# Optimization experiments

Measured on AMD Instinct MI355X. Metric: run time of the kernel, lower is better.

The kernel has to match this reference:

```python
import jax, jax.numpy as jnp
import numpy as np

B, L, D = 2, 4096, 1024      # batch, seq_len, d_model (expand_ratio=1 -> d_inner == D)
DS, RK, K = 16, 64, 3        # d_state, dt_rank, conv kernel size
EPS = 1e-5


def setup_inputs() -> dict:
    key = jax.random.key(0)
    ks = jax.random.split(key, 16)
    s = 0.02
    inp = {
        "x":      jax.random.normal(ks[0], (B, L, D), jnp.float32),
        "gamma":  jnp.ones((D,), jnp.float32),
        "beta":   jnp.zeros((D,), jnp.float32),
        "W_in":   jax.random.normal(ks[1], (D, 2 * D), jnp.float32) * s,
        "conv_w": jax.random.normal(ks[2], (K, 1, D), jnp.float32) * s,   # depthwise (k, 1, d)
        "conv_b": jnp.zeros((D,), jnp.float32),
        "W_xp":   jax.random.normal(ks[3], (D, RK), jnp.float32) * s,
        "W_Bg":   jax.random.normal(ks[4], (D, DS), jnp.float32) * s,
        "W_Cg":   jax.random.normal(ks[5], (D, DS), jnp.float32) * s,
        "W_dt":   jax.random.normal(ks[6], (RK, D), jnp.float32) * s,
        "b_dt":   jnp.zeros((D,), jnp.float32),
        "W_Bp":   jax.random.normal(ks[7], (DS, D), jnp.float32) * s,
        "W_Cp":   jax.random.normal(ks[8], (DS, D), jnp.float32) * s,
        "A":      -jnp.exp(jax.random.normal(ks[9], (D,), jnp.float32) * 0.5),  # negative for stability
        "D_skip": jnp.ones((D,), jnp.float32),
        "W_out":  jax.random.normal(ks[10], (D, D), jnp.float32) * s,
    }
    return inp


def reference(x, gamma, beta, W_in, conv_w, conv_b, W_xp, W_Bg, W_Cg,
              W_dt, b_dt, W_Bp, W_Cp, A, D_skip, W_out):
    d = x.shape[-1]
    # 1. LayerNorm
    mu = jnp.mean(x, -1, keepdims=True)
    var = jnp.mean(jnp.square(x - mu), -1, keepdims=True)
    xn = (x - mu) * jax.lax.rsqrt(var + EPS) * gamma + beta
    # 2. in_proj + split into main/gate branch
    xz = xn @ W_in                                 # (b, l, 2d)
    xb, z = jnp.split(xz, 2, axis=-1)
    # 3. depthwise Conv1D (same padding) + SiLU
    xc = jax.lax.conv_general_dilated(
        xb, conv_w, window_strides=(1,), padding='SAME',
        dimension_numbers=('NWC', 'WIO', 'NWC'), feature_group_count=d) + conv_b
    x_act = jax.nn.silu(xc)                        # (b, l, d)
    # SSM parameter generation
    delta = jax.nn.softplus((x_act @ W_xp) @ W_dt + b_dt)   # (b, l, d)
    Bm = (x_act @ W_Bg) @ W_Bp                     # (b, l, d)
    Cm = (x_act @ W_Cg) @ W_Cp                     # (b, l, d)
    # 4. diagonal selective scan: h_t = exp(delta*A)*h_{t-1} + delta*B*x ; y = C*h
    dA = jnp.exp(delta * A)
    dBx = delta * Bm * x_act
    def step(h, ab):
        a, bx = ab
        h = a * h + bx
        return h, h
    h0 = jnp.zeros_like(dA[:, 0])
    _, hs = jax.lax.scan(step, h0, (dA.transpose(1, 0, 2), dBx.transpose(1, 0, 2)))
    y = Cm * hs.transpose(1, 0, 2)
    # 5. skip-D, gating, out_proj + residual
    out_ssm = y + x_act * D_skip
    gated = out_ssm * jax.nn.silu(z)
    return gated @ W_out + x
```

## Files before the change

kernel.cpp:

```cpp
#include <hip/hip_runtime.h>
#include <math.h>

#define BB 2
#define LL 4096
#define DD 1024
#define DS 16
#define RK 64
#define MM (BB*LL)
#define NC 128
#define LC (LL/NC)

typedef __attribute__((ext_vector_type(8))) short short8;
typedef __attribute__((ext_vector_type(4))) float f32x4;

__device__ __forceinline__ unsigned short f2bf(float f) {
    union { float f; unsigned u; } v; v.f = f;
    unsigned r = v.u + 0x7fff + ((v.u >> 16) & 1);
    return (unsigned short)(r >> 16);
}
__device__ __forceinline__ float bf2f(unsigned short u) {
    union { unsigned u; float f; } v; v.u = ((unsigned)u) << 16;
    return v.f;
}
__device__ __forceinline__ float2 bf2x2(unsigned u) {
    return make_float2(bf2f((unsigned short)u), bf2f((unsigned short)(u >> 16)));
}
__device__ __forceinline__ unsigned f2bfx2(float lo, float hi) {
    return (unsigned)f2bf(lo) | ((unsigned)f2bf(hi) << 16);
}
__device__ __forceinline__ float fast_rcp(float x) {
    return __builtin_amdgcn_rcpf(x);
}
__device__ __forceinline__ float silu_f(float v) {
    return v * fast_rcp(1.0f + __expf(-v));
}
__device__ __forceinline__ void gload16(const void* g, void* l) {
    __builtin_amdgcn_global_load_lds(
        (const __attribute__((address_space(1))) unsigned int*)g,
        (__attribute__((address_space(3))) unsigned int*)l, 16, 0, 0);
}

__global__ __launch_bounds__(256)
void prep_misc(const float* __restrict__ W_in, const float* __restrict__ W_out,
               const float* __restrict__ W_xp, const float* __restrict__ W_Bg,
               const float* __restrict__ W_Cg, const float* __restrict__ W_dt,
               const float* __restrict__ W_Bp, const float* __restrict__ W_Cp,
               unsigned short* __restrict__ WinT, unsigned short* __restrict__ WoutT,
               unsigned short* __restrict__ WgT, unsigned short* __restrict__ WdtT,
               float* __restrict__ WBpT, float* __restrict__ WCpT,
               const float* __restrict__ x, const float* __restrict__ gamma,
               const float* __restrict__ beta, unsigned short* __restrict__ xn_bf) {
    __shared__ float t[32][33];
    __shared__ float ss[4], qq[4];
    int b = blockIdx.x;
    if (b >= 4224) {
        int row = b - 4224;
        int tid = threadIdx.x;
        const float4* xr = (const float4*)(x + (size_t)row * DD);
        float4 v = xr[tid];
        float s = v.x + v.y + v.z + v.w;
        float q = v.x*v.x + v.y*v.y + v.z*v.z + v.w*v.w;
        #pragma unroll
        for (int off = 32; off > 0; off >>= 1) {
            s += __shfl_down(s, off);
            q += __shfl_down(q, off);
        }
        int wv = tid >> 6;
        if ((tid & 63) == 0) { ss[wv] = s; qq[wv] = q; }
        __syncthreads();
        float S = ss[0] + ss[1] + ss[2] + ss[3];
        float Q = qq[0] + qq[1] + qq[2] + qq[3];
        float mu  = S * (1.0f / DD);
        float var = Q * (1.0f / DD) - mu * mu;
        float r = rsqrtf(var + 1e-5f);
        int d0 = tid * 4;
        float4 gv = *(const float4*)(gamma + d0);
        float4 bv = *(const float4*)(beta + d0);
        ushort4 o;
        o.x = f2bf((v.x - mu) * r * gv.x + bv.x);
        o.y = f2bf((v.y - mu) * r * gv.y + bv.y);
        o.z = f2bf((v.z - mu) * r * gv.z + bv.z);
        o.w = f2bf((v.w - mu) * r * gv.w + bv.w);
        *(ushort4*)&xn_bf[(size_t)row * DD + d0] = o;
    } else if (b < 3072) {
        const float* W; unsigned short* WT; int K, N, n0, k0;
        if (b < 2048) { W = W_in;  WT = WinT;  K = DD; N = 2 * DD;
                        n0 = (b & 63) * 32; k0 = (b >> 6) * 32; }
        else { int bb = b - 2048; W = W_out; WT = WoutT; K = DD; N = DD;
               n0 = (bb & 31) * 32; k0 = (bb >> 5) * 32; }
        int tx = threadIdx.x & 31, ty = threadIdx.x >> 5;
        #pragma unroll
        for (int r = 0; r < 32; r += 8)
            t[ty + r][tx] = W[(size_t)(k0 + ty + r) * N + n0 + tx];
        __syncthreads();
        #pragma unroll
        for (int r = 0; r < 32; r += 8) {
            int nl = ty + r;
            WT[(size_t)(n0 + nl) * K + k0 + tx] = f2bf(t[tx][nl]);
        }
    } else if (b < 3584) {
        int idx = (b - 3072) * 256 + threadIdx.x;
        int k = idx & 1023, n = idx >> 10;
        float v = 0.0f;
        if (n < 64)       v = W_xp[k * RK + n];
        else if (n < 80)  v = W_Bg[k * DS + (n - 64)];
        else if (n < 96)  v = W_Cg[k * DS + (n - 80)];
        WgT[idx] = f2bf(v);
    } else if (b < 4096) {
        int idx = (b - 3584) * 256 + threadIdx.x;
        int k = idx & 127, n = idx >> 7;
        float v = (k < 64) ? W_dt[k * 1024 + n] : 0.0f;
        WdtT[idx] = f2bf(v);
    } else if (b < 4160) {
        int idx = (b - 4096) * 256 + threadIdx.x;
        WBpT[idx] = W_Bp[(idx & 15) * 1024 + (idx >> 4)];
    } else {
        int idx = (b - 4160) * 256 + threadIdx.x;
        WCpT[idx] = W_Cp[(idx & 15) * 1024 + (idx >> 4)];
    }
}

#define MF(a, b, c) __builtin_amdgcn_mfma_f32_16x16x32_bf16(a, b, c, 0, 0, 0)
template<int EPI, int BM>
__global__ __launch_bounds__(512, 1)
void gemm256(const unsigned short* __restrict__ A, const unsigned short* __restrict__ BT,
             void* __restrict__ C0v, void* __restrict__ C1v,
             const float* __restrict__ res, int M, int N, int K) {
    constexpr int MR = BM / 32;
    constexpr int RA = BM / 64;
    constexpr int ABUF = BM * 64;
    extern __shared__ unsigned short sm[];
    unsigned short* As = sm;
    unsigned short* Bs = sm + 2 * ABUF;
    const int tid = threadIdx.x;
    const int wave = tid >> 6, lane = tid & 63;
    const int wr = wave >> 2, wc = wave & 3;
    const int fr = lane & 15, fs = lane >> 4;

    int nbx = gridDim.x;
    int nwg = nbx * gridDim.y;
    int bid = blockIdx.y * nbx + blockIdx.x;
    int cpx = nwg >> 3;
    int swz = (bid & 7) * cpx + (bid >> 3);
    int by = swz / nbx, bx = swz - by * nbx;
    size_t rb = (size_t)by * BM, cb = (size_t)bx * 256;

    const int srow = tid >> 3;
    const int ssw  = (tid & 7) ^ (srow & 7);
    const unsigned short* gA = A + (rb + srow) * K + ssw * 8;
    const unsigned short* gB = BT + (cb + srow) * K + ssw * 8;
    const size_t rstep = (size_t)64 * K;
    unsigned short* dA = As + tid * 8;
    unsigned short* dB = Bs + tid * 8;
    const int T = K >> 6;

#define STGA(rnd, buf, kt) gload16(gA + (size_t)(rnd) * rstep + (size_t)(kt) * 64, dA + (buf) * ABUF + (rnd) * 4096)
#define STGB(rnd, buf, kt) gload16(gB + (size_t)(rnd) * rstep + (size_t)(kt) * 64, dB + (buf) * 16384 + (rnd) * 4096)
#define FOFF(r, S) (((r) << 6) + ((((S) ^ ((r) & 7))) << 3))
#define LDA(i, kk) (*(const short8*)&Ab[FOFF(arow0 + ((i) << 4), fs + ((kk) << 2))])
#define LDB(j, kk) (*(const short8*)&Bb[FOFF(brow0 + ((j) << 4), fs + ((kk) << 2))])

    const int arow0 = wr * (BM / 2) + fr;
    const int brow0 = wc * 64 + fr;

    f32x4 acc[MR][4] = {};

    #pragma unroll
    for (int r = 0; r < RA; ++r) STGA(r, 0, 0);
    #pragma unroll
    for (int r = 0; r < 4; ++r) STGB(r, 0, 0);

    #pragma unroll 1
    for (int t = 0; t < T; ++t) {
        const int cur = t & 1, nx = cur ^ 1;
        const bool pf = (t + 1) < T;
        const unsigned short* Ab = As + cur * ABUF;
        const unsigned short* Bb = Bs + cur * 16384;

        if (pf) { STGA(0, nx, t + 1); STGB(0, nx, t + 1); }
        if (pf) { asm volatile("s_waitcnt vmcnt(2)" ::: "memory"); }
        else    { asm volatile("s_waitcnt vmcnt(0)" ::: "memory"); }
        __builtin_amdgcn_s_barrier();
        __builtin_amdgcn_sched_barrier(0);

        short8 bfr[4][2];
        #pragma unroll
        for (int j = 0; j < 4; ++j) {
            bfr[j][0] = LDB(j, 0);
            bfr[j][1] = LDB(j, 1);
        }
        __builtin_amdgcn_s_setprio(1);
        #pragma unroll
        for (int ii = 0; ii < MR / 4; ++ii) {
            short8 a0 = LDA(ii, 0), a1 = LDA(ii, 1);
            #pragma unroll
            for (int j = 0; j < 4; ++j) {
                acc[ii][j] = MF(a0, bfr[j][0], acc[ii][j]);
                acc[ii][j] = MF(a1, bfr[j][1], acc[ii][j]);
            }
        }
        __builtin_amdgcn_s_setprio(0);
        __builtin_amdgcn_sched_barrier(0);

        #pragma unroll
        for (int p = 1; p < 4; ++p) {
            if (pf) {
                if (p < RA) STGA(p, nx, t + 1);
                STGB(p, nx, t + 1);
            }
            __builtin_amdgcn_s_setprio(1);
            #pragma unroll
            for (int ii = 0; ii < MR / 4; ++ii) {
                const int i = p * (MR / 4) + ii;
                short8 a0 = LDA(i, 0), a1 = LDA(i, 1);
                #pragma unroll
                for (int j = 0; j < 4; ++j) {
                    acc[i][j] = MF(a0, bfr[j][0], acc[i][j]);
                    acc[i][j] = MF(a1, bfr[j][1], acc[i][j]);
                }
            }
            __builtin_amdgcn_s_setprio(0);
            __builtin_amdgcn_sched_barrier(0);
        }
        __builtin_amdgcn_s_barrier();
    }

    const int row0 = (int)rb + wr * (BM / 2) + fs * 4;
    const int col0 = (int)cb + wc * 64 + fr;
    if (EPI == 1) {
        unsigned short* Cd = (cb < DD) ? (unsigned short*)C0v : (unsigned short*)C1v;
        const int cadj = (cb < DD) ? 0 : -DD;
        #pragma unroll
        for (int i = 0; i < MR; ++i)
            #pragma unroll
            for (int j = 0; j < 4; ++j) {
                int col = col0 + cadj + (j << 4);
                #pragma unroll
                for (int q = 0; q < 4; ++q)
                    Cd[(size_t)(row0 + (i << 4) + q) * DD + col] = f2bf(acc[i][j][q]);
            }
    } else {
        float* C0 = (float*)C0v;
        #pragma unroll
        for (int i = 0; i < MR; ++i)
            #pragma unroll
            for (int j = 0; j < 4; ++j) {
                int col = col0 + (j << 4);
                #pragma unroll
                for (int q = 0; q < 4; ++q) {
                    size_t off = (size_t)(row0 + (i << 4) + q) * N + col;
                    C0[off] = acc[i][j][q] + res[off];
                }
            }
    }
#undef STGA
#undef STGB
#undef FOFF
#undef LDA
#undef LDB
}

__global__ __launch_bounds__(256)
void gemm_up(const unsigned short* __restrict__ A, const unsigned short* __restrict__ BT,
             unsigned short* __restrict__ C, const float* __restrict__ bias, int N) {
    __shared__ unsigned short As[128 * 128];
    __shared__ unsigned short Bs[128 * 128];
    int tid = threadIdx.x;
    int rb = blockIdx.y * 128, cb = blockIdx.x * 128;
    int wave = tid >> 6, lane = tid & 63;
    int wr = wave >> 1, wc = wave & 1;
    int fr = lane & 15, fs = lane >> 4;

    int srow16 = tid >> 4, sseg = tid & 15;
    #pragma unroll
    for (int r = 0; r < 8; ++r) {
        int row = r * 16 + srow16;
        int ss = sseg ^ (row & 15);
        gload16(A + (size_t)(rb + row) * 128 + ss * 8, (char*)As + r * 4096 + tid * 16);
        gload16(BT + (size_t)(cb + row) * 128 + ss * 8, (char*)Bs + r * 4096 + tid * 16);
    }
    asm volatile("s_waitcnt vmcnt(0)" ::: "memory");
    __syncthreads();

    f32x4 acc[4][4] = {};
    #pragma unroll
    for (int kk = 0; kk < 4; ++kk) {
        short8 af[4], bfr[4];
        #pragma unroll
        for (int i = 0; i < 4; ++i) {
            int row = (wr << 6) + (i << 4) + fr;
            int s = (fs + (kk << 2)) ^ (row & 15);
            af[i] = *(const short8*)&As[row * 128 + s * 8];
        }
        #pragma unroll
        for (int j = 0; j < 4; ++j) {
            int row = (wc << 6) + (j << 4) + fr;
            int s = (fs + (kk << 2)) ^ (row & 15);
            bfr[j] = *(const short8*)&Bs[row * 128 + s * 8];
        }
        #pragma unroll
        for (int i = 0; i < 4; ++i)
            #pragma unroll
            for (int j = 0; j < 4; ++j)
                acc[i][j] = MF(af[i], bfr[j], acc[i][j]);
    }

    int row0 = rb + (wr << 6) + (fs << 2);
    int col0 = (wc << 6) + fr;
    #pragma unroll
    for (int i = 0; i < 4; ++i)
        #pragma unroll
        for (int j = 0; j < 4; ++j) {
            int col = cb + col0 + (j << 4);
            float bv = bias[col];
            #pragma unroll
            for (int q = 0; q < 4; ++q) {
                float v = acc[i][j][q] + bv;
                v = fmaxf(v, 0.0f) + __logf(1.0f + __expf(-fabsf(v)));
                C[(size_t)(row0 + (i << 4) + q) * N + col] = f2bf(v);
            }
        }
}

__global__ __launch_bounds__(256)
void gemm_down(const unsigned short* __restrict__ A, const unsigned short* __restrict__ BT,
               unsigned short* __restrict__ C0, int M, int N, int K) {
    __shared__ unsigned short As[128 * 32];
    __shared__ unsigned short Bs[128 * 32];
    int tid = threadIdx.x;
    int rb = blockIdx.y * 128, cb = blockIdx.x * 128;
    int wave = tid >> 6, lane = tid & 63;
    int wr = wave >> 1, wc = wave & 1;
    int fr = lane & 15, fs = lane >> 4;

    int r0 = tid >> 2, s0 = tid & 3;
    int sw0 = s0 ^ ((r0 >> 1) & 3);
    const unsigned short* gA = A + (size_t)(rb + r0) * K + sw0 * 8;
    const unsigned short* gB = BT + (size_t)(cb + r0) * K + sw0 * 8;
    size_t half = (size_t)64 * K;
    char* lA0 = (char*)As + tid * 16;
    char* lA1 = (char*)As + (tid + 256) * 16;
    char* lB0 = (char*)Bs + tid * 16;
    char* lB1 = (char*)Bs + (tid + 256) * 16;

    int kb = blockIdx.z * (K >> 2), ke = kb + (K >> 2);

    f32x4 acc[4][4] = {};

    #pragma unroll 1
    for (int k0 = kb; k0 < ke; k0 += 32) {
        __syncthreads();
        gload16(gA + k0, lA0);
        gload16(gA + half + k0, lA1);
        gload16(gB + k0, lB0);
        gload16(gB + half + k0, lB1);
        __syncthreads();

        short8 af[4], bfr[4];
        #pragma unroll
        for (int i = 0; i < 4; i++) {
            int row = (wr << 6) + (i << 4) + fr;
            int off = (row << 5) + ((fs ^ ((row >> 1) & 3)) << 3);
            af[i] = *(const short8*)&As[off];
        }
        #pragma unroll
        for (int j = 0; j < 4; j++) {
            int row = (wc << 6) + (j << 4) + fr;
            int off = (row << 5) + ((fs ^ ((row >> 1) & 3)) << 3);
            bfr[j] = *(const short8*)&Bs[off];
        }
        #pragma unroll
        for (int i = 0; i < 4; i++)
            #pragma unroll
            for (int j = 0; j < 4; j++)
                acc[i][j] = MF(af[i], bfr[j], acc[i][j]);
    }

    int row0 = rb + (wr << 6) + (fs << 2);
    int col0 = (wc << 6) + fr;
    unsigned short* Cp = C0 + (size_t)blockIdx.z * M * N;
    #pragma unroll
    for (int i = 0; i < 4; i++)
        #pragma unroll
        for (int j = 0; j < 4; j++) {
            int col = cb + col0 + (j << 4);
            #pragma unroll
            for (int q = 0; q < 4; q++)
                Cp[(size_t)(row0 + (i << 4) + q) * N + col] = f2bf(acc[i][j][q]);
        }
}

__global__ __launch_bounds__(256)
void reduce_t(const unsigned short* __restrict__ tp, unsigned short* __restrict__ t_bf) {
    int idx = blockIdx.x * 256 + threadIdx.x;
    const size_t Q = (size_t)MM * 128;
    ushort4 a = ((const ushort4*)tp)[idx];
    ushort4 b = ((const ushort4*)(tp + Q))[idx];
    ushort4 c = ((const ushort4*)(tp + 2 * Q))[idx];
    ushort4 d = ((const ushort4*)(tp + 3 * Q))[idx];
    ushort4 o;
    o.x = f2bf(bf2f(a.x) + bf2f(b.x) + bf2f(c.x) + bf2f(d.x));
    o.y = f2bf(bf2f(a.y) + bf2f(b.y) + bf2f(c.y) + bf2f(d.y));
    o.z = f2bf(bf2f(a.z) + bf2f(b.z) + bf2f(c.z) + bf2f(d.z));
    o.w = f2bf(bf2f(a.w) + bf2f(b.w) + bf2f(c.w) + bf2f(d.w));
    ((ushort4*)t_bf)[idx] = o;
}

__global__ __launch_bounds__(256)
void conv_silu(const unsigned short* __restrict__ xb, const float* __restrict__ cw,
               const float* __restrict__ cb, unsigned short* __restrict__ xact) {
    int bid = blockIdx.x;
    int cpx = gridDim.x >> 3;
    int swz = (bid & 7) * cpx + (bid >> 3);
    int idx8 = swz * 256 + threadIdx.x;
    size_t e = (size_t)idx8 * 8;
    int d0 = (int)(e & (DD - 1));
    int bl = (int)(e >> 10);
    int l = bl & (LL - 1);
    short8 cur = *(const short8*)&xb[e];
    short8 prv = {}, nxt = {};
    if (l > 0)      prv = *(const short8*)&xb[e - DD];
    if (l < LL - 1) nxt = *(const short8*)&xb[e + DD];
    short8 o;
    #pragma unroll
    for (int j = 0; j < 8; j++) {
        int d = d0 + j;
        float acc = cb[d];
        acc = fmaf(bf2f((unsigned short)prv[j]), cw[0 * DD + d], acc);
        acc = fmaf(bf2f((unsigned short)cur[j]), cw[1 * DD + d], acc);
        acc = fmaf(bf2f((unsigned short)nxt[j]), cw[2 * DD + d], acc);
        o[j] = (short)f2bf(silu_f(acc));
    }
    *(short8*)&xact[e] = o;
}

__global__ __launch_bounds__(256)
void scan_p1(const unsigned short* __restrict__ delta, const unsigned short* __restrict__ xact,
             const unsigned short* __restrict__ t_bf, const float* __restrict__ WBpT,
             const float* __restrict__ A, float* __restrict__ P, float* __restrict__ Hc) {
    __shared__ float tbs[LC][16];
    int tid = threadIdx.x;
    int d = (blockIdx.x * 256 + tid) * 2;
    int c = blockIdx.y, b = blockIdx.z;
    int row0 = b * LL + c * LC;
    {
        int rr = tid >> 3, kp = (tid & 7) * 2;
        float2 f = bf2x2(*(const unsigned*)&t_bf[(size_t)(row0 + rr) * 128 + 64 + kp]);
        tbs[rr][kp] = f.x; tbs[rr][kp + 1] = f.y;
    }
    __syncthreads();
    float wB0[16], wB1[16];
    #pragma unroll
    for (int j = 0; j < 4; ++j) {
        *(float4*)&wB0[j * 4] = *(const float4*)&WBpT[(size_t)d * 16 + j * 4];
        *(float4*)&wB1[j * 4] = *(const float4*)&WBpT[(size_t)(d + 1) * 16 + j * 4];
    }
    float2 a_d = *(const float2*)&A[d];
    float h0 = 0.0f, h1 = 0.0f, sd0 = 0.0f, sd1 = 0.0f;
    #pragma unroll 4
    for (int i = 0; i < LC; i++) {
        size_t o = (size_t)(row0 + i) * DD + d;
        float2 dl = bf2x2(*(const unsigned*)&delta[o]);
        float2 xa = bf2x2(*(const unsigned*)&xact[o]);
        float bm0 = 0.0f, bm1 = 0.0f;
        #pragma unroll
        for (int j = 0; j < 4; ++j) {
            float4 t4 = *(const float4*)&tbs[i][j * 4];
            bm0 = fmaf(t4.x, wB0[j*4+0], bm0); bm1 = fmaf(t4.x, wB1[j*4+0], bm1);
            bm0 = fmaf(t4.y, wB0[j*4+1], bm0); bm1 = fmaf(t4.y, wB1[j*4+1], bm1);
            bm0 = fmaf(t4.z, wB0[j*4+2], bm0); bm1 = fmaf(t4.z, wB1[j*4+2], bm1);
            bm0 = fmaf(t4.w, wB0[j*4+3], bm0); bm1 = fmaf(t4.w, wB1[j*4+3], bm1);
        }
        float a0 = __expf(dl.x * a_d.x);
        float a1 = __expf(dl.y * a_d.y);
        h0 = fmaf(a0, h0, dl.x * bm0 * xa.x);
        h1 = fmaf(a1, h1, dl.y * bm1 * xa.y);
        sd0 += dl.x; sd1 += dl.y;
    }
    int pc = (b * NC + c) * DD + d;
    *(float2*)&P[pc]  = make_float2(__expf(a_d.x * sd0), __expf(a_d.y * sd1));
    *(float2*)&Hc[pc] = make_float2(h0, h1);
}

__global__ __launch_bounds__(256)
void scan_p2(const float* __restrict__ P, const float* __restrict__ Hc,
             float* __restrict__ hin) {
    extern __shared__ float sP[];
    float* sH = sP + NC * 128;
    int b = blockIdx.y;
    int d0 = blockIdx.x * 128;
    for (int idx = threadIdx.x; idx < NC * 128; idx += 256) {
        int c = idx >> 7, dd = idx & 127;
        int o = (b * NC + c) * DD + d0 + dd;
        sP[idx] = P[o];
        sH[idx] = Hc[o];
    }
    __syncthreads();
    if (threadIdx.x < 128) {
        int dd = threadIdx.x;
        float carry = 0.0f;
        #pragma unroll 4
        for (int c = 0; c < NC; ++c) {
            float pv = sP[c * 128 + dd];
            float hv = sH[c * 128 + dd];
            sP[c * 128 + dd] = carry;
            carry = fmaf(pv, carry, hv);
        }
    }
    __syncthreads();
    for (int idx = threadIdx.x; idx < NC * 128; idx += 256) {
        int c = idx >> 7, dd = idx & 127;
        hin[(b * NC + c) * DD + d0 + dd] = sP[idx];
    }
}

__global__ __launch_bounds__(256)
void scan_p3(const unsigned short* __restrict__ delta, const unsigned short* __restrict__ xact,
             const unsigned short* __restrict__ zb, const unsigned short* __restrict__ t_bf,
             const float* __restrict__ WBpT, const float* __restrict__ WCpT,
             const float* __restrict__ hin, const float* __restrict__ A,
             const float* __restrict__ Dsk, unsigned short* __restrict__ g) {
    __shared__ float tbs[LC][16];
    __shared__ float tcs[LC][16];
    int tid = threadIdx.x;
    int d = (blockIdx.x * 256 + tid) * 2;
    int c = blockIdx.y, b = blockIdx.z;
    int row0 = b * LL + c * LC;
    {
        int rr = tid >> 3, kp = (tid & 7) * 2;
        const unsigned short* tr = &t_bf[(size_t)(row0 + rr) * 128];
        float2 fb = bf2x2(*(const unsigned*)&tr[64 + kp]);
        float2 fc = bf2x2(*(const unsigned*)&tr[80 + kp]);
        tbs[rr][kp] = fb.x; tbs[rr][kp + 1] = fb.y;
        tcs[rr][kp] = fc.x; tcs[rr][kp + 1] = fc.y;
    }
    __syncthreads();
    float wB0[16], wB1[16], wC0[16], wC1[16];
    #pragma unroll
    for (int j = 0; j < 4; ++j) {
        *(float4*)&wB0[j * 4] = *(const float4*)&WBpT[(size_t)d * 16 + j * 4];
        *(float4*)&wB1[j * 4] = *(const float4*)&WBpT[(size_t)(d + 1) * 16 + j * 4];
        *(float4*)&wC0[j * 4] = *(const float4*)&WCpT[(size_t)d * 16 + j * 4];
        *(float4*)&wC1[j * 4] = *(const float4*)&WCpT[(size_t)(d + 1) * 16 + j * 4];
    }
    float2 a_d = *(const float2*)&A[d];
    float2 dsk = *(const float2*)&Dsk[d];
    float2 hv = *(const float2*)&hin[(b * NC + c) * DD + d];
    float h0 = hv.x, h1 = hv.y;
    #pragma unroll 4
    for (int i = 0; i < LC; i++) {
        size_t o = (size_t)(row0 + i) * DD + d;
        float2 dl = bf2x2(*(const unsigned*)&delta[o]);
        float2 xa = bf2x2(*(const unsigned*)&xact[o]);
        float2 zv = bf2x2(*(const unsigned*)&zb[o]);
        float bm0 = 0.0f, bm1 = 0.0f, cm0 = 0.0f, cm1 = 0.0f;
        #pragma unroll
        for (int j = 0; j < 4; ++j) {
            float4 t4 = *(const float4*)&tbs[i][j * 4];
            float4 c4 = *(const float4*)&tcs[i][j * 4];
            bm0 = fmaf(t4.x, wB0[j*4+0], bm0); bm1 = fmaf(t4.x, wB1[j*4+0], bm1);
            bm0 = fmaf(t4.y, wB0[j*4+1], bm0); bm1 = fmaf(t4.y, wB1[j*4+1], bm1);
            bm0 = fmaf(t4.z, wB0[j*4+2], bm0); bm1 = fmaf(t4.z, wB1[j*4+2], bm1);
            bm0 = fmaf(t4.w, wB0[j*4+3], bm0); bm1 = fmaf(t4.w, wB1[j*4+3], bm1);
            cm0 = fmaf(c4.x, wC0[j*4+0], cm0); cm1 = fmaf(c4.x, wC1[j*4+0], cm1);
            cm0 = fmaf(c4.y, wC0[j*4+1], cm0); cm1 = fmaf(c4.y, wC1[j*4+1], cm1);
            cm0 = fmaf(c4.z, wC0[j*4+2], cm0); cm1 = fmaf(c4.z, wC1[j*4+2], cm1);
            cm0 = fmaf(c4.w, wC0[j*4+3], cm0); cm1 = fmaf(c4.w, wC1[j*4+3], cm1);
        }
        float a0 = __expf(dl.x * a_d.x);
        float a1 = __expf(dl.y * a_d.y);
        h0 = fmaf(a0, h0, dl.x * bm0 * xa.x);
        h1 = fmaf(a1, h1, dl.y * bm1 * xa.y);
        float os0 = fmaf(xa.x, dsk.x, cm0 * h0);
        float os1 = fmaf(xa.y, dsk.y, cm1 * h1);
        float g0 = os0 * silu_f(zv.x);
        float g1 = os1 * silu_f(zv.y);
        *(unsigned*)&g[o] = f2bfx2(g0, g1);
    }
}

extern "C" void kernel_launch(void* const* d_in, const int* in_sizes, int n_in,
                              void* d_out, int out_size, void* d_ws, size_t ws_size,
                              hipStream_t stream) {
    const float* x      = (const float*)d_in[0];
    const float* gamma  = (const float*)d_in[1];
    const float* beta   = (const float*)d_in[2];
    const float* W_in   = (const float*)d_in[3];
    const float* conv_w = (const float*)d_in[4];
    const float* conv_b = (const float*)d_in[5];
    const float* W_xp   = (const float*)d_in[6];
    const float* W_Bg   = (const float*)d_in[7];
    const float* W_Cg   = (const float*)d_in[8];
    const float* W_dt   = (const float*)d_in[9];
    const float* b_dt   = (const float*)d_in[10];
    const float* W_Bp   = (const float*)d_in[11];
    const float* W_Cp   = (const float*)d_in[12];
    const float* A      = (const float*)d_in[13];
    const float* Dsk    = (const float*)d_in[14];
    const float* W_out  = (const float*)d_in[15];
    float* out = (float*)d_out;

    const size_t BIG = (size_t)MM * DD;
    char* p = (char*)d_ws;
    unsigned short* xn_bf   = (unsigned short*)p;  p += BIG * 2;
    unsigned short* xb_bf   = (unsigned short*)p;  p += BIG * 2;
    unsigned short* z_bf    = (unsigned short*)p;  p += BIG * 2;
    unsigned short* xact_bf = (unsigned short*)p;  p += BIG * 2;
    unsigned short* delta_bf= (unsigned short*)p;  p += BIG * 2;
    unsigned short* t_bf    = (unsigned short*)p;  p += (size_t)MM * 128 * 2;
    unsigned short* tpart   = (unsigned short*)p;  p += (size_t)4 * MM * 128 * 2;
    float* P     = (float*)p;                      p += (size_t)BB * NC * DD * 4;
    float* Hc    = (float*)p;                      p += (size_t)BB * NC * DD * 4;
    float* hin   = (float*)p;                      p += (size_t)BB * NC * DD * 4;
    unsigned short* WinT  = (unsigned short*)p;    p += (size_t)2 * DD * DD * 2;
    unsigned short* WoutT = (unsigned short*)p;    p += (size_t)DD * DD * 2;
    unsigned short* WgT   = (unsigned short*)p;    p += (size_t)128 * DD * 2;
    unsigned short* WdtT  = (unsigned short*)p;    p += (size_t)DD * 128 * 2;
    float* WBpT = (float*)p;                       p += (size_t)DD * 16 * 4;
    float* WCpT = (float*)p;                       p += (size_t)DD * 16 * 4;
    unsigned short* g_bf  = xn_bf;

    {
        void (*k1)(const unsigned short*, const unsigned short*, void*, void*,
                   const float*, int, int, int) = gemm256<1, 256>;
        void (*k2)(const unsigned short*, const unsigned short*, void*, void*,
                   const float*, int, int, int) = gemm256<2, 128>;
        void (*k3)(const float*, const float*, float*) = scan_p2;
        (void)hipFuncSetAttribute((const void*)k1,
            hipFuncAttributeMaxDynamicSharedMemorySize, 131072);
        (void)hipFuncSetAttribute((const void*)k2,
            hipFuncAttributeMaxDynamicSharedMemorySize, 98304);
        (void)hipFuncSetAttribute((const void*)k3,
            hipFuncAttributeMaxDynamicSharedMemorySize, 131072);
    }

    prep_misc<<<4224 + MM, 256, 0, stream>>>(W_in, W_out, W_xp, W_Bg, W_Cg,
                                             W_dt, W_Bp, W_Cp,
                                             WinT, WoutT, WgT, WdtT, WBpT, WCpT,
                                             x, gamma, beta, xn_bf);
    gemm256<1, 256><<<dim3(2 * DD / 256, MM / 256), 512, 131072, stream>>>(
        xn_bf, WinT, xb_bf, z_bf, nullptr, MM, 2 * DD, DD);
    conv_silu<<<(MM * DD / 8) / 256, 256, 0, stream>>>(xb_bf, conv_w, conv_b, xact_bf);
    gemm_down<<<dim3(1, MM / 128, 4), 256, 0, stream>>>(
        xact_bf, WgT, tpart, MM, 128, DD);
    reduce_t<<<(MM * 128 / 4) / 256, 256, 0, stream>>>(tpart, t_bf);
    gemm_up<<<dim3(DD / 128, MM / 128), 256, 0, stream>>>(
        t_bf, WdtT, delta_bf, b_dt, DD);
    scan_p1<<<dim3(DD / 512, NC, BB), 256, 0, stream>>>(delta_bf, xact_bf, t_bf,
                                                        WBpT, A, P, Hc);
    scan_p2<<<dim3(DD / 128, BB), 256, 131072, stream>>>(P, Hc, hin);
    scan_p3<<<dim3(DD / 512, NC, BB), 256, 0, stream>>>(delta_bf, xact_bf, z_bf, t_bf,
                                                        WBpT, WCpT, hin, A, Dsk, g_bf);
    gemm256<2, 128><<<dim3(DD / 256, MM / 128), 512, 98304, stream>>>(
        g_bf, WoutT, out, nullptr, x, MM, DD, DD);
}
```

Before: 156.7 us.

## Fuse down-projection, split-K reduction and dt up-projection into one kernel

Replaces the three kernels gemm_down (split-K over 4), reduce_t and gemm_up with a single gemm_param kernel. Each block computes a 128-row tile of the x_act·[W_xp|W_Bg|W_Cg] product over the full K, keeps it in shared memory as bf16, and writes only the B/C columns to global memory. It then loops over eight 128-column tiles of W_dt to produce softplus(delta) directly. This removes the partial-sum buffer traffic, the reduction pass and two launches. In exchange the grid shrinks to 64 blocks, which leaves most CUs idle and serialises the up-projection work inside each block.

```diff
diff --git a/kernel.cpp b/kernel.cpp
--- a/kernel.cpp
+++ b/kernel.cpp
@@ -261,94 +261,34 @@
 }
 
 __global__ __launch_bounds__(256)
-void gemm_up(const unsigned short* __restrict__ A, const unsigned short* __restrict__ BT,
-             unsigned short* __restrict__ C, const float* __restrict__ bias, int N) {
-    __shared__ unsigned short As[128 * 128];
-    __shared__ unsigned short Bs[128 * 128];
+void gemm_param(const unsigned short* __restrict__ xact, const unsigned short* __restrict__ WgT,
+                const unsigned short* __restrict__ WdtT, const float* __restrict__ bias,
+                unsigned short* __restrict__ t_out, unsigned short* __restrict__ delta) {
+    extern __shared__ unsigned short sm[];
+    unsigned short* As = sm;
+    unsigned short* Bs = sm + 4096;
+    unsigned short* tL = sm + 8192;
+    unsigned short* B2 = sm + 24576;
     int tid = threadIdx.x;
-    int rb = blockIdx.y * 128, cb = blockIdx.x * 128;
+    int rb = blockIdx.x * 128;
     int wave = tid >> 6, lane = tid & 63;
     int wr = wave >> 1, wc = wave & 1;
     int fr = lane & 15, fs = lane >> 4;
 
-    int srow16 = tid >> 4, sseg = tid & 15;
-    #pragma unroll
-    for (int r = 0; r < 8; ++r) {
-        int row = r * 16 + srow16;
-        int ss = sseg ^ (row & 15);
-        gload16(A + (size_t)(rb + row) * 128 + ss * 8, (char*)As + r * 4096 + tid * 16);
-        gload16(BT + (size_t)(cb + row) * 128 + ss * 8, (char*)Bs + r * 4096 + tid * 16);
-    }
-    asm volatile("s_waitcnt vmcnt(0)" ::: "memory");
-    __syncthreads();
-
-    f32x4 acc[4][4] = {};
-    #pragma unroll
-    for (int kk = 0; kk < 4; ++kk) {
-        short8 af[4], bfr[4];
-        #pragma unroll
-        for (int i = 0; i < 4; ++i) {
-            int row = (wr << 6) + (i << 4) + fr;
-            int s = (fs + (kk << 2)) ^ (row & 15);
-            af[i] = *(const short8*)&As[row * 128 + s * 8];
-        }
-        #pragma unroll
-        for (int j = 0; j < 4; ++j) {
-            int row = (wc << 6) + (j << 4) + fr;
-            int s = (fs + (kk << 2)) ^ (row & 15);
-            bfr[j] = *(const short8*)&Bs[row * 128 + s * 8];
-        }
-        #pragma unroll
-        for (int i = 0; i < 4; ++i)
-            #pragma unroll
-            for (int j = 0; j < 4; ++j)
-                acc[i][j] = MF(af[i], bfr[j], acc[i][j]);
-    }
-
-    int row0 = rb + (wr << 6) + (fs << 2);
-    int col0 = (wc << 6) + fr;
-    #pragma unroll
-    for (int i = 0; i < 4; ++i)
-        #pragma unroll
-        for (int j = 0; j < 4; ++j) {
-            int col = cb + col0 + (j << 4);
-            float bv = bias[col];
-            #pragma unroll
-            for (int q = 0; q < 4; ++q) {
-                float v = acc[i][j][q] + bv;
-                v = fmaxf(v, 0.0f) + __logf(1.0f + __expf(-fabsf(v)));
-                C[(size_t)(row0 + (i << 4) + q) * N + col] = f2bf(v);
-            }
-        }
-}
-
-__global__ __launch_bounds__(256)
-void gemm_down(const unsigned short* __restrict__ A, const unsigned short* __restrict__ BT,
-               unsigned short* __restrict__ C0, int M, int N, int K) {
-    __shared__ unsigned short As[128 * 32];
-    __shared__ unsigned short Bs[128 * 32];
-    int tid = threadIdx.x;
-    int rb = blockIdx.y * 128, cb = blockIdx.x * 128;
-    int wave = tid >> 6, lane = tid & 63;
-    int wr = wave >> 1, wc = wave & 1;
-    int fr = lane & 15, fs = lane >> 4;
-
     int r0 = tid >> 2, s0 = tid & 3;
     int sw0 = s0 ^ ((r0 >> 1) & 3);
-    const unsigned short* gA = A + (size_t)(rb + r0) * K + sw0 * 8;
-    const unsigned short* gB = BT + (size_t)(cb + r0) * K + sw0 * 8;
-    size_t half = (size_t)64 * K;
+    const unsigned short* gA = xact + (size_t)(rb + r0) * DD + sw0 * 8;
+    const unsigned short* gB = WgT + (size_t)r0 * DD + sw0 * 8;
+    size_t half = (size_t)64 * DD;
     char* lA0 = (char*)As + tid * 16;
     char* lA1 = (char*)As + (tid + 256) * 16;
     char* lB0 = (char*)Bs + tid * 16;
     char* lB1 = (char*)Bs + (tid + 256) * 16;
 
-    int kb = blockIdx.z * (K >> 2), ke = kb + (K >> 2);
-
     f32x4 acc[4][4] = {};
 
     #pragma unroll 1
-    for (int k0 = kb; k0 < ke; k0 += 32) {
+    for (int k0 = 0; k0 < DD; k0 += 32) {
         __syncthreads();
         gload16(gA + k0, lA0);
         gload16(gA + half + k0, lA1);
@@ -376,34 +316,80 @@
                 acc[i][j] = MF(af[i], bfr[j], acc[i][j]);
     }
 
-    int row0 = rb + (wr << 6) + (fs << 2);
-    int col0 = (wc << 6) + fr;
-    unsigned short* Cp = C0 + (size_t)blockIdx.z * M * N;
-    #pragma unroll
-    for (int i = 0; i < 4; i++)
-        #pragma unroll
-        for (int j = 0; j < 4; j++) {
-            int col = cb + col0 + (j << 4);
-            #pragma unroll
-            for (int q = 0; q < 4; q++)
-                Cp[(size_t)(row0 + (i << 4) + q) * N + col] = f2bf(acc[i][j][q]);
-        }
-}
-
-__global__ __launch_bounds__(256)
-void reduce_t(const unsigned short* __restrict__ tp, unsigned short* __restrict__ t_bf) {
-    int idx = blockIdx.x * 256 + threadIdx.x;
-    const size_t Q = (size_t)MM * 128;
-    ushort4 a = ((const ushort4*)tp)[idx];
-    ushort4 b = ((const ushort4*)(tp + Q))[idx];
-    ushort4 c = ((const ushort4*)(tp + 2 * Q))[idx];
-    ushort4 d = ((const ushort4*)(tp + 3 * Q))[idx];
-    ushort4 o;
-    o.x = f2bf(bf2f(a.x) + bf2f(b.x) + bf2f(c.x) + bf2f(d.x));
-    o.y = f2bf(bf2f(a.y) + bf2f(b.y) + bf2f(c.y) + bf2f(d.y));
-    o.z = f2bf(bf2f(a.z) + bf2f(b.z) + bf2f(c.z) + bf2f(d.z));
-    o.w = f2bf(bf2f(a.w) + bf2f(b.w) + bf2f(c.w) + bf2f(d.w));
-    ((ushort4*)t_bf)[idx] = o;
+    __syncthreads();
+    {
+        int row0l = (wr << 6) + (fs << 2);
+        int col0l = (wc << 6) + fr;
+        #pragma unroll
+        for (int i = 0; i < 4; i++)
+            #pragma unroll
+            for (int j = 0; j < 4; j++) {
+                int col = col0l + (j << 4);
+                int seg = col >> 3, off = col & 7;
+                #pragma unroll
+                for (int q = 0; q < 4; q++) {
+                    int row = row0l + (i << 4) + q;
+                    unsigned short bv = f2bf(acc[i][j][q]);
+                    tL[row * 128 + ((seg ^ (row & 15)) << 3) + off] = bv;
+                    if (col >= 64 && col < 96)
+                        t_out[(size_t)(rb + row) * 128 + col] = bv;
+                }
+            }
+    }
+
+    int srow16 = tid >> 4, sseg = tid & 15;
+    #pragma unroll 1
+    for (int ct = 0; ct < 8; ++ct) {
+        __syncthreads();
+        #pragma unroll
+        for (int r = 0; r < 8; ++r) {
+            int row = r * 16 + srow16;
+            int ss = sseg ^ (row & 15);
+            gload16(WdtT + (size_t)(ct * 128 + row) * 128 + ss * 8,
+                    (char*)B2 + r * 4096 + tid * 16);
+        }
+        asm volatile("s_waitcnt vmcnt(0)" ::: "memory");
+        __syncthreads();
+
+        f32x4 acc2[4][4] = {};
+        #pragma unroll
+        for (int kk = 0; kk < 4; ++kk) {
+            short8 af[4], bfr[4];
+            #pragma unroll
+            for (int i = 0; i < 4; ++i) {
+                int row = (wr << 6) + (i << 4) + fr;
+                int s = (fs + (kk << 2)) ^ (row & 15);
+                af[i] = *(const short8*)&tL[row * 128 + s * 8];
+            }
+            #pragma unroll
+            for (int j = 0; j < 4; ++j) {
+                int row = (wc << 6) + (j << 4) + fr;
+                int s = (fs + (kk << 2)) ^ (row & 15);
+                bfr[j] = *(const short8*)&B2[row * 128 + s * 8];
+            }
+            #pragma unroll
+            for (int i = 0; i < 4; ++i)
+                #pragma unroll
+                for (int j = 0; j < 4; ++j)
+                    acc2[i][j] = MF(af[i], bfr[j], acc2[i][j]);
+        }
+
+        int row0l = rb + (wr << 6) + (fs << 2);
+        int col0l = ct * 128 + (wc << 6) + fr;
+        #pragma unroll
+        for (int i = 0; i < 4; ++i)
+            #pragma unroll
+            for (int j = 0; j < 4; ++j) {
+                int col = col0l + (j << 4);
+                float bv = bias[col];
+                #pragma unroll
+                for (int q = 0; q < 4; ++q) {
+                    float v = acc2[i][j][q] + bv;
+                    v = fmaxf(v, 0.0f) + __logf(1.0f + __expf(-fabsf(v)));
+                    delta[(size_t)(row0l + (i << 4) + q) * DD + col] = f2bf(v);
+                }
+            }
+    }
 }
 
 __global__ __launch_bounds__(256)
@@ -608,7 +594,6 @@
     unsigned short* xact_bf = (unsigned short*)p;  p += BIG * 2;
     unsigned short* delta_bf= (unsigned short*)p;  p += BIG * 2;
     unsigned short* t_bf    = (unsigned short*)p;  p += (size_t)MM * 128 * 2;
-    unsigned short* tpart   = (unsigned short*)p;  p += (size_t)4 * MM * 128 * 2;
     float* P     = (float*)p;                      p += (size_t)BB * NC * DD * 4;
     float* Hc    = (float*)p;                      p += (size_t)BB * NC * DD * 4;
     float* hin   = (float*)p;                      p += (size_t)BB * NC * DD * 4;
@@ -626,12 +611,16 @@
         void (*k2)(const unsigned short*, const unsigned short*, void*, void*,
                    const float*, int, int, int) = gemm256<2, 128>;
         void (*k3)(const float*, const float*, float*) = scan_p2;
+        void (*k4)(const unsigned short*, const unsigned short*, const unsigned short*,
+                   const float*, unsigned short*, unsigned short*) = gemm_param;
         (void)hipFuncSetAttribute((const void*)k1,
             hipFuncAttributeMaxDynamicSharedMemorySize, 131072);
         (void)hipFuncSetAttribute((const void*)k2,
             hipFuncAttributeMaxDynamicSharedMemorySize, 98304);
         (void)hipFuncSetAttribute((const void*)k3,
             hipFuncAttributeMaxDynamicSharedMemorySize, 131072);
+        (void)hipFuncSetAttribute((const void*)k4,
+            hipFuncAttributeMaxDynamicSharedMemorySize, 81920);
     }
 
     prep_misc<<<4224 + MM, 256, 0, stream>>>(W_in, W_out, W_xp, W_Bg, W_Cg,
@@ -641,11 +630,8 @@
     gemm256<1, 256><<<dim3(2 * DD / 256, MM / 256), 512, 131072, stream>>>(
         xn_bf, WinT, xb_bf, z_bf, nullptr, MM, 2 * DD, DD);
     conv_silu<<<(MM * DD / 8) / 256, 256, 0, stream>>>(xb_bf, conv_w, conv_b, xact_bf);
-    gemm_down<<<dim3(1, MM / 128, 4), 256, 0, stream>>>(
-        xact_bf, WgT, tpart, MM, 128, DD);
-    reduce_t<<<(MM * 128 / 4) / 256, 256, 0, stream>>>(tpart, t_bf);
-    gemm_up<<<dim3(DD / 128, MM / 128), 256, 0, stream>>>(
-        t_bf, WdtT, delta_bf, b_dt, DD);
+    gemm_param<<<MM / 128, 256, 81920, stream>>>(xact_bf, WgT, WdtT, b_dt,
+                                                 t_bf, delta_bf);
     scan_p1<<<dim3(DD / 512, NC, BB), 256, 0, stream>>>(delta_bf, xact_bf, t_bf,
                                                         WBpT, A, P, Hc);
     scan_p2<<<dim3(DD / 128, BB), 256, 131072, stream>>>(P, Hc, hin);
```

After: 210.4 us. +34.2%, slower.
